# Kernel tuning notes

Measured on AMD Instinct MI355X. Metric: run time of the kernel, lower is better.

## Reference

```python
import jax, jax.numpy as jnp
import numpy as np

B, T, N = 16, 1024, 128
WIN, STEP = 30, 2
MOMENT_ORDERS = (2, 4, 8)
D_MODEL = 256


def _mask_diag(corr):
    n = corr.shape[-1]
    eye = jnp.eye(n, dtype=corr.dtype)
    return corr * (1.0 - eye) + eye


def corrcoef_time(xw):
    # xw: [..., L, N] -> corr over channels: [..., N, N]
    L = xw.shape[-2]
    xm = xw - xw.mean(axis=-2, keepdims=True)
    cov = jnp.einsum('...ln,...lm->...nm', xm, xm) / (L - 1 + 1e-8)
    var = jnp.clip(jnp.diagonal(cov, axis1=-2, axis2=-1), 1e-8, None)
    std = jnp.sqrt(var)
    corr = cov / (std[..., :, None] * std[..., None, :])
    corr = jnp.nan_to_num(corr, nan=0.0, posinf=0.0, neginf=0.0)
    return _mask_diag(corr)


def rowwise_corr(M):
    # M: [B, N, F]
    Xc = M - M.mean(axis=-1, keepdims=True)
    num = jnp.einsum('bnf,bmf->bnm', Xc, Xc)
    den1 = jnp.sqrt(jnp.clip((Xc ** 2).sum(axis=-1), 1e-8, None))
    corr = num / (den1[:, :, None] * den1[:, None, :])
    corr = jnp.nan_to_num(corr, nan=0.0, posinf=0.0, neginf=0.0)
    return _mask_diag(corr)


def layer_norm(x, gamma, beta, eps=1e-5):
    mu = x.mean(axis=-1, keepdims=True)
    var = ((x - mu) ** 2).mean(axis=-1, keepdims=True)
    return (x - mu) / jnp.sqrt(var + eps) * gamma + beta


def normalize_adj(adj):
    n = adj.shape[-1]
    A_hat = adj + jnp.eye(n, dtype=adj.dtype)
    d = A_hat.sum(axis=-1)
    dis = jnp.sqrt(1.0 / jnp.clip(d, 1e-8, None))
    return A_hat * dis[:, :, None] * dis[:, None, :]


def setup_inputs() -> dict:
    key = jax.random.key(0)
    ks = jax.random.split(key, 8)
    in_dim = len(MOMENT_ORDERS) * N
    return {
        'x': jax.random.normal(ks[0], (B, T, N), dtype=jnp.float32),
        'ln_gamma': jnp.ones((in_dim,), jnp.float32),
        'ln_beta': jnp.zeros((in_dim,), jnp.float32),
        'W1': jax.random.normal(ks[1], (in_dim, D_MODEL), jnp.float32) * 0.05,
        'b1': jnp.zeros((D_MODEL,), jnp.float32),
        'W2': jax.random.normal(ks[2], (D_MODEL, D_MODEL), jnp.float32) * 0.05,
        'b2': jnp.zeros((D_MODEL,), jnp.float32),
        'Wc': jax.random.normal(ks[3], (D_MODEL, 1), jnp.float32) * 0.05,
        'bc': jnp.zeros((1,), jnp.float32),
    }


def reference(x, ln_gamma, ln_beta, W1, b1, W2, b2, Wc, bc):
    # sliding windows (static indices)
    starts = np.arange(0, T - WIN + 1, STEP)
    idx = starts[:, None] + np.arange(WIN)[None, :]
    xw = x[:, idx, :]
    lo = corrcoef_time(xw)                            # [B, Wn, N, N]

    mean_lo = lo.mean(axis=1, keepdims=True)
    centered = lo - mean_lo
    cm_list, ho_list = [], []
    for d in MOMENT_ORDERS:
        cm = jnp.nan_to_num((centered ** d).mean(axis=1),
                            nan=0.0, posinf=0.0, neginf=0.0)  # [B, N, N]
        cm_list.append(cm)
        ho_list.append(rowwise_corr(cm))

    X = jnp.concatenate(cm_list, axis=-1)             # [B, N, 3N]
    X = layer_norm(X, ln_gamma, ln_beta)

    A = jnp.stack(ho_list, axis=1).mean(axis=1)
    A = 0.5 * (A + jnp.swapaxes(A, 1, 2))
    A_norm = normalize_adj(A)

    H = jax.nn.relu(jnp.einsum('bnm,bmd->bnd', A_norm, X @ W1 + b1))
    H = jax.nn.relu(jnp.einsum('bnm,bmd->bnd', A_norm, H @ W2 + b2))
    g = H.mean(axis=1)                                # [B, d_model]
    out = jax.nn.sigmoid(g @ Wc + bc)                 # [B, 1]
    return out
```

## Files before the change

kernel.cpp:

```cpp
#include <hip/hip_runtime.h>
#include <math.h>

#define BB  16
#define TT  1024
#define NN  128
#define WIN 30
#define NWD 498
#define DM  256
#define IND 384
#define GW  9

#define INV_W (1.0f/498.0f)

#define SARR (BB*NN*NN)

#define OFF_A     0
#define OFF_G     (OFF_A    + BB*NWD*NN)
#define OFF_CM2   (OFF_G    + BB*NWD*NN)
#define OFF_CM4   (OFF_CM2  + SARR)
#define OFF_CM8   (OFF_CM4  + SARR)
#define OFF_AD    (OFF_CM8  + SARR)
#define OFF_PART  (OFF_AD   + 3*SARR)
#define OFF_ANORM OFF_PART
#define OFF_BUFA  (OFF_ANORM + SARR)
#define OFF_BUFB  (OFF_BUFA + BB*NN*DM)

__global__ __launch_bounds__(128) void k1_stats(const float* __restrict__ x, float* __restrict__ ws) {
    int bx = blockIdx.x;
    int c = bx & 15, b = bx >> 4;
    int w0 = c*32, w1 = min(NWD, w0+32);
    int n = threadIdx.x;
    const float* xp = x + (size_t)b*TT*NN + n;

    float sum = 0.f, sq = 0.f;
    for (int t = 2*w0; t < 2*w0 + WIN; ++t) {
        float v = xp[(size_t)t*NN];
        sum += v; sq = fmaf(v, v, sq);
    }
    for (int w = w0; w < w1; ++w) {
        if (w > w0) {
            float o0 = xp[(size_t)(2*w-2)*NN], o1 = xp[(size_t)(2*w-1)*NN];
            float n0 = xp[(size_t)(2*w+28)*NN], n1 = xp[(size_t)(2*w+29)*NN];
            sum += (n0 + n1) - (o0 + o1);
            sq  += (n0*n0 + n1*n1) - (o0*o0 + o1*o1);
        }
        float mean = sum * (1.0f/30.0f);
        float ss = sq - 30.0f*mean*mean;
        float var = fmaxf(ss * (1.0f/29.0f), 1e-8f);
        float a = (1.0f / sqrtf(var)) * 0.185695338f;
        ws[OFF_A + ((size_t)b*NWD + w)*NN + n] = a;
        ws[OFF_G + ((size_t)b*NWD + w)*NN + n] = mean * a * 5.477225575f;
    }
}

__global__ __launch_bounds__(256) __attribute__((amdgpu_waves_per_eu(3, 3)))
void k24_inc(const float* __restrict__ x, float* __restrict__ ws) {
    __shared__ __align__(16) float xr[64][NN];
    __shared__ __align__(16) float sa[GW][NN];
    __shared__ __align__(16) float sg[GW][NN];
    int bx = blockIdx.x;
    int wc = bx & 7;
    int slab = (bx >> 3) % 6;
    int b = bx / 48;
    const char IS[6] = {0,0,0,0,1,1};
    const char JS[6] = {0,1,2,3,2,3};
    int is = IS[slab], js = JS[slab];
    int w0 = wc * 63, w1 = min(NWD, w0 + 63);
    int tid = threadIdx.x;
    int jg = tid & 7, ig = tid >> 3;
    int i0 = is*64 + ig*2;
    int j0 = js*32 + jg*4;

    const float* xb = x + (size_t)b*TT*NN;
    const float* Ab = ws + OFF_A + (size_t)b*NWD*NN;
    const float* Gb = ws + OFF_G + (size_t)b*NWD*NN;

    float P[2][4];
    float S1[2][4], S2[2][4], S3[2][4], S4[2][4], S5[2][4], S6[2][4], S7[2][4], S8[2][4];
#pragma unroll
    for (int p=0;p<2;++p)
#pragma unroll
        for (int q=0;q<4;++q) {
            P[p][q]=0.f;
            S1[p][q]=0.f;S2[p][q]=0.f;S3[p][q]=0.f;S4[p][q]=0.f;
            S5[p][q]=0.f;S6[p][q]=0.f;S7[p][q]=0.f;S8[p][q]=0.f;
        }

    auto moments = [&](int k) {
        float2 ai = *(const float2*)&sa[k][i0];
        float2 gi = *(const float2*)&sg[k][i0];
        float4 aj = *(const float4*)&sa[k][j0];
        float4 gj = *(const float4*)&sg[k][j0];
        float av[2] = {ai.x, ai.y};
        float mg[2] = {-gi.x, -gi.y};
        float aw[4] = {aj.x, aj.y, aj.z, aj.w};
        float gw[4] = {gj.x, gj.y, gj.z, gj.w};
#pragma unroll
        for (int p=0;p<2;++p)
#pragma unroll
            for (int q=0;q<4;++q) {
                float aa  = av[p]*aw[q];
                float ngg = mg[p]*gw[q];
                float c   = fmaf(P[p][q], aa, ngg);
                float c2 = c*c;
                float c3 = c2*c;
                float c4 = c2*c2;
                S1[p][q] += c;
                S2[p][q] += c2;
                S3[p][q] += c3;
                S4[p][q] += c4;
                S5[p][q] = fmaf(c4, c,  S5[p][q]);
                S6[p][q] = fmaf(c3, c3, S6[p][q]);
                S7[p][q] = fmaf(c3, c4, S7[p][q]);
                S8[p][q] = fmaf(c4, c4, S8[p][q]);
            }
    };

    int rlo = 2*w0;
    for (int wg = w0; wg < w1; wg += GW) {
        int m = min(GW, w1 - wg);
        __syncthreads();
        int rhi = 2*(wg + m - 1) + 29;
        int nr = rhi - rlo + 1;
        for (int idx = tid; idx < nr*32; idx += 256) {
            int r = idx >> 5, c4 = idx & 31;
            int t = rlo + r;
            *(float4*)&xr[t & 63][c4*4] = ((const float4*)(xb + (size_t)t*NN))[c4];
        }
        for (int idx = tid; idx < m*32; idx += 256) {
            int k = idx >> 5, c4 = idx & 31;
            *(float4*)&sa[k][c4*4] = ((const float4*)(Ab + (size_t)(wg+k)*NN))[c4];
        }
        for (int idx = tid; idx < m*32; idx += 256) {
            int k = idx >> 5, c4 = idx & 31;
            *(float4*)&sg[k][c4*4] = ((const float4*)(Gb + (size_t)(wg+k)*NN))[c4];
        }
        rlo = rhi + 1;
        __syncthreads();

        int kstart = 0;
        if (wg == w0) {
#pragma unroll 6
            for (int k = 0; k < WIN; ++k) {
                int t = 2*w0 + k;
                float2 xi = *(const float2*)&xr[t & 63][i0];
                float4 xj = *(const float4*)&xr[t & 63][j0];
                float av[2] = {xi.x, xi.y};
                float bv[4] = {xj.x, xj.y, xj.z, xj.w};
#pragma unroll
                for (int p=0;p<2;++p)
#pragma unroll
                    for (int q=0;q<4;++q) P[p][q] = fmaf(av[p], bv[q], P[p][q]);
            }
            moments(0);
            kstart = 1;
        }
        for (int k = kstart; k < m; ++k) {
            int w = wg + k;
            int tr[4] = {2*w - 2, 2*w - 1, 2*w + 28, 2*w + 29};
#pragma unroll
            for (int kk = 0; kk < 4; ++kk) {
                int t = tr[kk];
                float sgn = (kk < 2) ? -1.0f : 1.0f;
                float2 xi = *(const float2*)&xr[t & 63][i0];
                float4 xj = *(const float4*)&xr[t & 63][j0];
                float av[2] = {sgn*xi.x, sgn*xi.y};
                float bv[4] = {xj.x, xj.y, xj.z, xj.w};
#pragma unroll
                for (int p=0;p<2;++p)
#pragma unroll
                    for (int q=0;q<4;++q) P[p][q] = fmaf(av[p], bv[q], P[p][q]);
            }
            moments(k);
        }
    }

    float* tp = ws + OFF_PART + (size_t)bx*16384 + tid*8;
#define STORE_ARR(A, S) \
    *(float4*)&tp[(A)*2048]     = make_float4(S[0][0], S[0][1], S[0][2], S[0][3]); \
    *(float4*)&tp[(A)*2048 + 4] = make_float4(S[1][0], S[1][1], S[1][2], S[1][3]);
    STORE_ARR(0, S1) STORE_ARR(1, S2) STORE_ARR(2, S3) STORE_ARR(3, S4)
    STORE_ARR(4, S5) STORE_ARR(5, S6) STORE_ARR(6, S7) STORE_ARR(7, S8)
#undef STORE_ARR
}

__global__ __launch_bounds__(256) void kred(float* __restrict__ ws) {
    int pair = blockIdx.x >> 3, sub = blockIdx.x & 7;
    int b = pair / 6, slab = pair % 6;
    const char IS[6] = {0,0,0,0,1,1};
    const char JS[6] = {0,1,2,3,2,3};
    int is = IS[slab], js = JS[slab];
    int off = sub*256 + threadIdx.x;
    const float* base = ws + OFF_PART + (size_t)(b*48 + slab*8)*16384;

    float E[8];
#pragma unroll
    for (int a=0;a<8;++a) E[a] = 0.f;
    for (int c = 0; c < 8; ++c) {
        const float* tp = base + (size_t)c*16384;
#pragma unroll
        for (int a=0;a<8;++a) E[a] += tp[a*2048 + off];
    }

    int tid_old = off >> 3, e = off & 7;
    int ig = tid_old >> 3, jg = tid_old & 7;
    int p = e >> 2, q = e & 3;
    int i = is*64 + ig*2 + p;
    int j = js*32 + jg*4 + q;

    float cm2, cm4, cm8;
    if (i == j) {
        cm2 = 0.f; cm4 = 0.f; cm8 = 0.f;
    } else {
        float e1 = E[0]*INV_W, e2 = E[1]*INV_W, e3 = E[2]*INV_W, e4 = E[3]*INV_W;
        float e5 = E[4]*INV_W, e6 = E[5]*INV_W, e7 = E[6]*INV_W, e8 = E[7]*INV_W;
        float m  = e1;
        float m2 = m*m, m3 = m2*m, m4 = m2*m2, m5 = m4*m, m6 = m3*m3, m8 = m4*m4;
        cm2 = e2 - m2;
        cm4 = e4 - 4.f*m*e3 + 6.f*m2*e2 - 3.f*m4;
        cm8 = e8 - 8.f*m*e7 + 28.f*m2*e6 - 56.f*m3*e5 + 70.f*m4*e4
                 - 56.f*m5*e3 + 28.f*m6*e2 - 7.f*m8;
    }
    float* C2 = ws + OFF_CM2 + (size_t)b*NN*NN;
    float* C4 = ws + OFF_CM4 + (size_t)b*NN*NN;
    float* C8 = ws + OFF_CM8 + (size_t)b*NN*NN;
    C2[i*NN + j] = cm2; C2[j*NN + i] = cm2;
    C4[i*NN + j] = cm4; C4[j*NN + i] = cm4;
    C8[i*NN + j] = cm8; C8[j*NN + i] = cm8;
}

__global__ __launch_bounds__(256) void kB(const float* __restrict__ gamma, const float* __restrict__ beta,
                                          const float* __restrict__ W1, const float* __restrict__ b1,
                                          float* __restrict__ ws) {
    __shared__ __align__(16) float smem[NN*(NN+1) + 2*NN];
    int blk = blockIdx.x, tid = threadIdx.x;
    if (blk < 192) {
        int rem = blk % 12;
        int b = blk / 12, di = rem >> 2, jq = rem & 3;
        float* Xc  = smem;
        float* rmn = smem + NN*(NN+1);
        float* iden = rmn + NN;
        const float* cm = ws + (di==0 ? OFF_CM2 : (di==1 ? OFF_CM4 : OFF_CM8)) + (size_t)b*NN*NN;
        for (int idx = tid; idx < NN*NN; idx += 256) {
            int n = idx >> 7, f = idx & 127;
            Xc[n*(NN+1)+f] = cm[idx];
        }
        __syncthreads();
        if (tid < NN) {
            float s = 0.f;
            for (int f = 0; f < NN; ++f) s += Xc[tid*(NN+1)+f];
            rmn[tid] = s * (1.0f/NN);
        }
        __syncthreads();
        for (int idx = tid; idx < NN*NN; idx += 256) {
            int n = idx >> 7, f = idx & 127;
            Xc[n*(NN+1)+f] -= rmn[n];
        }
        __syncthreads();
        if (tid < NN) {
            float s = 0.f;
            for (int f = 0; f < NN; ++f) { float v = Xc[tid*(NN+1)+f]; s = fmaf(v, v, s); }
            iden[tid] = 1.0f/sqrtf(fmaxf(s, 1e-8f));
        }
        __syncthreads();
        int n0 = (tid >> 4)*8, m0 = jq*32 + (tid & 15)*2;
        float acc[8][2];
#pragma unroll
        for (int k=0;k<8;++k) { acc[k][0]=0.f; acc[k][1]=0.f; }
        for (int f = 0; f < NN; ++f) {
            float am0 = Xc[(m0  )*(NN+1)+f];
            float am1 = Xc[(m0+1)*(NN+1)+f];
#pragma unroll
            for (int k=0;k<8;++k) {
                float an = Xc[(n0+k)*(NN+1)+f];
                acc[k][0] = fmaf(an, am0, acc[k][0]);
                acc[k][1] = fmaf(an, am1, acc[k][1]);
            }
        }
        float* Ad = ws + OFF_AD + (size_t)(b*3 + di)*NN*NN;
#pragma unroll
        for (int k=0;k<8;++k)
#pragma unroll
            for (int l=0;l<2;++l) {
                int gi = n0+k, gj = m0+l;
                float v = acc[k][l]*iden[gi]*iden[gj];
                if (gi == gj) v = 1.0f;
                Ad[gi*NN + gj] = v;
            }
    } else {
        int r0 = (blk - 192) * 8;
        float* Xs = smem;
        float* sm = smem + 8*IND;
        float* sr = sm + 8;
        for (int r = 0; r < 8; ++r) {
            int row = r0 + r;
            int b = row >> 7, n = row & 127;
            const float* c2 = ws + OFF_CM2 + ((size_t)b*NN + n)*NN;
            const float* c4 = ws + OFF_CM4 + ((size_t)b*NN + n)*NN;
            const float* c8 = ws + OFF_CM8 + ((size_t)b*NN + n)*NN;
            for (int c = tid; c < IND; c += 256)
                Xs[r*IND+c] = (c < 128) ? c2[c] : (c < 256) ? c4[c-128] : c8[c-256];
        }
        __syncthreads();
        {
            int team = tid >> 5, lane = tid & 31;
            float s = 0.f;
            for (int c = lane; c < IND; c += 32) s += Xs[team*IND + c];
#pragma unroll
            for (int o = 16; o > 0; o >>= 1) s += __shfl_down(s, o, 32);
            float mean = __shfl(s, 0, 32) * (1.0f/IND);
            float v = 0.f;
            for (int c = lane; c < IND; c += 32) { float d = Xs[team*IND + c] - mean; v = fmaf(d, d, v); }
#pragma unroll
            for (int o = 16; o > 0; o >>= 1) v += __shfl_down(v, o, 32);
            if (lane == 0) {
                sm[team] = mean;
                sr[team] = 1.0f / sqrtf(v*(1.0f/IND) + 1e-5f);
            }
        }
        __syncthreads();
        for (int r = 0; r < 8; ++r) {
            float mean = sm[r], rstd = sr[r];
            for (int c = tid; c < IND; c += 256)
                Xs[r*IND+c] = (Xs[r*IND+c] - mean)*rstd*gamma[c] + beta[c];
        }
        __syncthreads();
        float acc[8];
        float bv = b1[tid];
#pragma unroll
        for (int r = 0; r < 8; ++r) acc[r] = bv;
#pragma unroll 4
        for (int k = 0; k < IND; ++k) {
            float wv = W1[(size_t)k*DM + tid];
#pragma unroll
            for (int r = 0; r < 8; ++r) acc[r] = fmaf(Xs[r*IND+k], wv, acc[r]);
        }
        float* O = ws + OFF_BUFA;
#pragma unroll
        for (int r = 0; r < 8; ++r) O[(size_t)(r0+r)*DM + tid] = acc[r];
    }
}

__global__ __launch_bounds__(256) void k6_anorm(float* __restrict__ ws) {
    __shared__ float As[NN][NN+1];
    __shared__ float dis[NN];
    int b = blockIdx.x;
    const float* A0 = ws + OFF_AD + (size_t)(b*3 + 0)*NN*NN;
    const float* A1 = ws + OFF_AD + (size_t)(b*3 + 1)*NN*NN;
    const float* A2 = ws + OFF_AD + (size_t)(b*3 + 2)*NN*NN;
    int tid = threadIdx.x;
    for (int idx = tid; idx < NN*NN; idx += 256) {
        int n = idx >> 7, m = idx & 127;
        int ji = m*NN + n;
        float s = A0[idx] + A0[ji] + A1[idx] + A1[ji] + A2[idx] + A2[ji];
        As[n][m] = s * (1.0f/6.0f);
    }
    __syncthreads();
    if (tid < NN) {
        float d = 1.0f;
        for (int m = 0; m < NN; ++m) d += As[tid][m];
        dis[tid] = sqrtf(1.0f / fmaxf(d, 1e-8f));
    }
    __syncthreads();
    float* An = ws + OFF_ANORM + (size_t)b*NN*NN;
    for (int idx = tid; idx < NN*NN; idx += 256) {
        int n = idx >> 7, m = idx & 127;
        float v = As[n][m] + (n==m ? 1.0f : 0.0f);
        An[idx] = v * dis[n] * dis[m];
    }
}

__global__ __launch_bounds__(256) void k98_propgemm(const float* __restrict__ W2, const float* __restrict__ b2,
                                                    float* __restrict__ ws) {
    __shared__ float Ar[8][NN];
    __shared__ float Hs[8][DM];
    int bx = blockIdx.x;
    int b = bx >> 4, n0 = (bx & 15)*8;
    int tid = threadIdx.x;
    const float* A = ws + OFF_ANORM + (size_t)b*NN*NN;
    if (tid < NN) {
#pragma unroll
        for (int r = 0; r < 8; ++r) Ar[r][tid] = A[(n0+r)*NN + tid];
    }
    __syncthreads();
    float acc[8] = {0,0,0,0,0,0,0,0};
    const float* Z = ws + OFF_BUFA + (size_t)b*NN*DM;
#pragma unroll 4
    for (int m = 0; m < NN; ++m) {
        float z = Z[(size_t)m*DM + tid];
#pragma unroll
        for (int r = 0; r < 8; ++r) acc[r] = fmaf(Ar[r][m], z, acc[r]);
    }
#pragma unroll
    for (int r = 0; r < 8; ++r) Hs[r][tid] = fmaxf(acc[r], 0.0f);
    __syncthreads();
    float acc2[8];
    float bv = b2[tid];
#pragma unroll
    for (int r = 0; r < 8; ++r) acc2[r] = bv;
#pragma unroll 4
    for (int k = 0; k < DM; ++k) {
        float wv = W2[(size_t)k*DM + tid];
#pragma unroll
        for (int r = 0; r < 8; ++r) acc2[r] = fmaf(Hs[r][k], wv, acc2[r]);
    }
    float* O = ws + OFF_BUFB + (size_t)b*NN*DM;
#pragma unroll
    for (int r = 0; r < 8; ++r) O[(size_t)(n0+r)*DM + tid] = acc2[r];
}

__global__ __launch_bounds__(256) void k9_prop(float* __restrict__ ws) {
    __shared__ float Ar[8][NN];
    int bx = blockIdx.x;
    int b = bx >> 4, n0 = (bx & 15)*8;
    int tid = threadIdx.x;
    const float* A = ws + OFF_ANORM + (size_t)b*NN*NN;
    if (tid < NN) {
#pragma unroll
        for (int r = 0; r < 8; ++r) Ar[r][tid] = A[(n0+r)*NN + tid];
    }
    __syncthreads();
    float acc[8] = {0,0,0,0,0,0,0,0};
    const float* Z = ws + OFF_BUFB + (size_t)b*NN*DM;
#pragma unroll 4
    for (int m = 0; m < NN; ++m) {
        float z = Z[(size_t)m*DM + tid];
#pragma unroll
        for (int r = 0; r < 8; ++r) acc[r] = fmaf(Ar[r][m], z, acc[r]);
    }
    float* O = ws + OFF_BUFA + (size_t)b*NN*DM;
#pragma unroll
    for (int r = 0; r < 8; ++r) O[(size_t)(n0+r)*DM + tid] = fmaxf(acc[r], 0.0f);
}

__global__ __launch_bounds__(256) void k12_head(const float* __restrict__ Wc, const float* __restrict__ bc,
                                                float* __restrict__ ws, float* __restrict__ outp) {
    __shared__ float red[256];
    int b = blockIdx.x, tid = threadIdx.x;
    const float* H = ws + OFF_BUFA + (size_t)b*NN*DM;
    float s = 0.f;
    for (int n = 0; n < NN; ++n) s += H[(size_t)n*DM + tid];
    red[tid] = s * (1.0f/NN) * Wc[tid];
    __syncthreads();
    for (int o = 128; o > 0; o >>= 1) { if (tid < o) red[tid] += red[tid+o]; __syncthreads(); }
    if (tid == 0) outp[b] = 1.0f/(1.0f + expf(-(red[0] + bc[0])));
}

extern "C" void kernel_launch(void* const* d_in, const int* in_sizes, int n_in,
                              void* d_out, int out_size, void* d_ws, size_t ws_size,
                              hipStream_t stream) {
    (void)in_sizes; (void)n_in; (void)out_size; (void)ws_size;
    const float* x     = (const float*)d_in[0];
    const float* gamma = (const float*)d_in[1];
    const float* beta  = (const float*)d_in[2];
    const float* W1    = (const float*)d_in[3];
    const float* b1    = (const float*)d_in[4];
    const float* W2    = (const float*)d_in[5];
    const float* b2    = (const float*)d_in[6];
    const float* Wc    = (const float*)d_in[7];
    const float* bc    = (const float*)d_in[8];
    float* ws  = (float*)d_ws;
    float* out = (float*)d_out;

    k1_stats   <<<BB*16,   128, 0, stream>>>(x, ws);
    k24_inc    <<<BB*6*8,  256, 0, stream>>>(x, ws);
    kred       <<<BB*6*8,  256, 0, stream>>>(ws);
    kB         <<<448,     256, 0, stream>>>(gamma, beta, W1, b1, ws);
    k6_anorm   <<<BB,      256, 0, stream>>>(ws);
    k98_propgemm<<<BB*16,  256, 0, stream>>>(W2, b2, ws);
    k9_prop    <<<BB*16,   256, 0, stream>>>(ws);
    k12_head   <<<BB,      256, 0, stream>>>(Wc, bc, ws, out);
}
```

Measured before the change: 264.1 us.

## Fuse reduction, anorm and head into producers via last-block-done atomic counters

Removes three kernel launches (kred, k6_anorm, k12_head) by having the last block to finish in each group, found through an atomic counter, perform the downstream reduction or epilogue. Counters are zeroed in k1_stats. This is meant to cut launch gaps and tail overhead between the small kernels. In exchange, the reduction, anorm and head work is serialized onto one block per group instead of being spread across many blocks, which can lengthen the tail. The scheme also depends on acquire/release atomics for memory visibility.

Result: slower. 305.4 us (+15.6%).

```diff
diff --git a/kernel.cpp b/kernel.cpp
--- a/kernel.cpp
+++ b/kernel.cpp
@@ -24,9 +24,11 @@
 #define OFF_ANORM OFF_PART
 #define OFF_BUFA  (OFF_ANORM + SARR)
 #define OFF_BUFB  (OFF_BUFA + BB*NN*DM)
+#define OFF_CTR   (OFF_PART + 768*16384)
 
 __global__ __launch_bounds__(128) void k1_stats(const float* __restrict__ x, float* __restrict__ ws) {
     int bx = blockIdx.x;
+    if (bx == 0 && threadIdx.x < 128) ((unsigned*)(ws + OFF_CTR))[threadIdx.x] = 0u;
     int c = bx & 15, b = bx >> 4;
     int w0 = c*32, w1 = min(NWD, w0+32);
     int n = threadIdx.x;
@@ -58,6 +60,7 @@
     __shared__ __align__(16) float xr[64][NN];
     __shared__ __align__(16) float sa[GW][NN];
     __shared__ __align__(16) float sg[GW][NN];
+    __shared__ unsigned iswin;
     int bx = blockIdx.x;
     int wc = bx & 7;
     int slab = (bx >> 3) % 6;
@@ -182,57 +185,59 @@
     STORE_ARR(0, S1) STORE_ARR(1, S2) STORE_ARR(2, S3) STORE_ARR(3, S4)
     STORE_ARR(4, S5) STORE_ARR(5, S6) STORE_ARR(6, S7) STORE_ARR(7, S8)
 #undef STORE_ARR
-}
-
-__global__ __launch_bounds__(256) void kred(float* __restrict__ ws) {
-    int pair = blockIdx.x >> 3, sub = blockIdx.x & 7;
-    int b = pair / 6, slab = pair % 6;
-    const char IS[6] = {0,0,0,0,1,1};
-    const char JS[6] = {0,1,2,3,2,3};
-    int is = IS[slab], js = JS[slab];
-    int off = sub*256 + threadIdx.x;
-    const float* base = ws + OFF_PART + (size_t)(b*48 + slab*8)*16384;
-
-    float E[8];
-#pragma unroll
-    for (int a=0;a<8;++a) E[a] = 0.f;
-    for (int c = 0; c < 8; ++c) {
-        const float* tp = base + (size_t)c*16384;
-#pragma unroll
-        for (int a=0;a<8;++a) E[a] += tp[a*2048 + off];
-    }
-
-    int tid_old = off >> 3, e = off & 7;
-    int ig = tid_old >> 3, jg = tid_old & 7;
-    int p = e >> 2, q = e & 3;
-    int i = is*64 + ig*2 + p;
-    int j = js*32 + jg*4 + q;
-
-    float cm2, cm4, cm8;
-    if (i == j) {
-        cm2 = 0.f; cm4 = 0.f; cm8 = 0.f;
-    } else {
-        float e1 = E[0]*INV_W, e2 = E[1]*INV_W, e3 = E[2]*INV_W, e4 = E[3]*INV_W;
-        float e5 = E[4]*INV_W, e6 = E[5]*INV_W, e7 = E[6]*INV_W, e8 = E[7]*INV_W;
-        float m  = e1;
-        float m2 = m*m, m3 = m2*m, m4 = m2*m2, m5 = m4*m, m6 = m3*m3, m8 = m4*m4;
-        cm2 = e2 - m2;
-        cm4 = e4 - 4.f*m*e3 + 6.f*m2*e2 - 3.f*m4;
-        cm8 = e8 - 8.f*m*e7 + 28.f*m2*e6 - 56.f*m3*e5 + 70.f*m4*e4
-                 - 56.f*m5*e3 + 28.f*m6*e2 - 7.f*m8;
-    }
-    float* C2 = ws + OFF_CM2 + (size_t)b*NN*NN;
-    float* C4 = ws + OFF_CM4 + (size_t)b*NN*NN;
-    float* C8 = ws + OFF_CM8 + (size_t)b*NN*NN;
-    C2[i*NN + j] = cm2; C2[j*NN + i] = cm2;
-    C4[i*NN + j] = cm4; C4[j*NN + i] = cm4;
-    C8[i*NN + j] = cm8; C8[j*NN + i] = cm8;
+
+    __syncthreads();
+    if (tid == 0) {
+        unsigned* ctr = (unsigned*)(ws + OFF_CTR);
+        unsigned old = __hip_atomic_fetch_add(&ctr[b*6 + slab], 1u,
+                                              __ATOMIC_ACQ_REL, __HIP_MEMORY_SCOPE_AGENT);
+        iswin = (old == 7u) ? 1u : 0u;
+    }
+    __syncthreads();
+    if (iswin) {
+        const float* base = ws + OFF_PART + (size_t)(b*48 + slab*8)*16384;
+        float* C2 = ws + OFF_CM2 + (size_t)b*NN*NN;
+        float* C4 = ws + OFF_CM4 + (size_t)b*NN*NN;
+        float* C8 = ws + OFF_CM8 + (size_t)b*NN*NN;
+        for (int k = 0; k < 8; ++k) {
+            int off = k*256 + tid;
+            float E[8];
+#pragma unroll
+            for (int a=0;a<8;++a) E[a] = 0.f;
+            for (int c = 0; c < 8; ++c) {
+                const float* tpp = base + (size_t)c*16384;
+#pragma unroll
+                for (int a=0;a<8;++a) E[a] += tpp[a*2048 + off];
+            }
+            int tid_old = off >> 3, e = off & 7;
+            int igo = tid_old >> 3, jgo = tid_old & 7;
+            int p = e >> 2, q = e & 3;
+            int i = is*64 + igo*2 + p;
+            int j = js*32 + jgo*4 + q;
+            float cm2, cm4, cm8;
+            if (i == j) { cm2 = 0.f; cm4 = 0.f; cm8 = 0.f; }
+            else {
+                float e1 = E[0]*INV_W, e2 = E[1]*INV_W, e3 = E[2]*INV_W, e4 = E[3]*INV_W;
+                float e5 = E[4]*INV_W, e6 = E[5]*INV_W, e7 = E[6]*INV_W, e8 = E[7]*INV_W;
+                float m  = e1;
+                float m2 = m*m, m3 = m2*m, m4 = m2*m2, m5 = m4*m, m6 = m3*m3, m8 = m4*m4;
+                cm2 = e2 - m2;
+                cm4 = e4 - 4.f*m*e3 + 6.f*m2*e2 - 3.f*m4;
+                cm8 = e8 - 8.f*m*e7 + 28.f*m2*e6 - 56.f*m3*e5 + 70.f*m4*e4
+                         - 56.f*m5*e3 + 28.f*m6*e2 - 7.f*m8;
+            }
+            C2[i*NN + j] = cm2; C2[j*NN + i] = cm2;
+            C4[i*NN + j] = cm4; C4[j*NN + i] = cm4;
+            C8[i*NN + j] = cm8; C8[j*NN + i] = cm8;
+        }
+    }
 }
 
 __global__ __launch_bounds__(256) void kB(const float* __restrict__ gamma, const float* __restrict__ beta,
                                           const float* __restrict__ W1, const float* __restrict__ b1,
                                           float* __restrict__ ws) {
     __shared__ __align__(16) float smem[NN*(NN+1) + 2*NN];
+    __shared__ unsigned winB;
     int blk = blockIdx.x, tid = threadIdx.x;
     if (blk < 192) {
         int rem = blk % 12;
@@ -287,6 +292,41 @@
                 if (gi == gj) v = 1.0f;
                 Ad[gi*NN + gj] = v;
             }
+
+        __syncthreads();
+        if (tid == 0) {
+            unsigned* ctr = (unsigned*)(ws + OFF_CTR);
+            unsigned old = __hip_atomic_fetch_add(&ctr[96 + b], 1u,
+                                                  __ATOMIC_ACQ_REL, __HIP_MEMORY_SCOPE_AGENT);
+            winB = (old == 11u) ? 1u : 0u;
+        }
+        __syncthreads();
+        if (winB) {
+            float* As = smem;
+            float* dis = smem + NN*(NN+1);
+            const float* A0 = ws + OFF_AD + (size_t)(b*3 + 0)*NN*NN;
+            const float* A1 = ws + OFF_AD + (size_t)(b*3 + 1)*NN*NN;
+            const float* A2 = ws + OFF_AD + (size_t)(b*3 + 2)*NN*NN;
+            for (int idx = tid; idx < NN*NN; idx += 256) {
+                int n = idx >> 7, m = idx & 127;
+                int ji = m*NN + n;
+                float s = A0[idx] + A0[ji] + A1[idx] + A1[ji] + A2[idx] + A2[ji];
+                As[n*(NN+1)+m] = s * (1.0f/6.0f);
+            }
+            __syncthreads();
+            if (tid < NN) {
+                float d = 1.0f;
+                for (int m = 0; m < NN; ++m) d += As[tid*(NN+1)+m];
+                dis[tid] = sqrtf(1.0f / fmaxf(d, 1e-8f));
+            }
+            __syncthreads();
+            float* An = ws + OFF_ANORM + (size_t)b*NN*NN;
+            for (int idx = tid; idx < NN*NN; idx += 256) {
+                int n = idx >> 7, m = idx & 127;
+                float v = As[n*(NN+1)+m] + (n==m ? 1.0f : 0.0f);
+                An[idx] = v * dis[n] * dis[m];
+            }
+        }
     } else {
         int r0 = (blk - 192) * 8;
         float* Xs = smem;
@@ -341,35 +381,6 @@
     }
 }
 
-__global__ __launch_bounds__(256) void k6_anorm(float* __restrict__ ws) {
-    __shared__ float As[NN][NN+1];
-    __shared__ float dis[NN];
-    int b = blockIdx.x;
-    const float* A0 = ws + OFF_AD + (size_t)(b*3 + 0)*NN*NN;
-    const float* A1 = ws + OFF_AD + (size_t)(b*3 + 1)*NN*NN;
-    const float* A2 = ws + OFF_AD + (size_t)(b*3 + 2)*NN*NN;
-    int tid = threadIdx.x;
-    for (int idx = tid; idx < NN*NN; idx += 256) {
-        int n = idx >> 7, m = idx & 127;
-        int ji = m*NN + n;
-        float s = A0[idx] + A0[ji] + A1[idx] + A1[ji] + A2[idx] + A2[ji];
-        As[n][m] = s * (1.0f/6.0f);
-    }
-    __syncthreads();
-    if (tid < NN) {
-        float d = 1.0f;
-        for (int m = 0; m < NN; ++m) d += As[tid][m];
-        dis[tid] = sqrtf(1.0f / fmaxf(d, 1e-8f));
-    }
-    __syncthreads();
-    float* An = ws + OFF_ANORM + (size_t)b*NN*NN;
-    for (int idx = tid; idx < NN*NN; idx += 256) {
-        int n = idx >> 7, m = idx & 127;
-        float v = As[n][m] + (n==m ? 1.0f : 0.0f);
-        An[idx] = v * dis[n] * dis[m];
-    }
-}
-
 __global__ __launch_bounds__(256) void k98_propgemm(const float* __restrict__ W2, const float* __restrict__ b2,
                                                     float* __restrict__ ws) {
     __shared__ float Ar[8][NN];
@@ -409,8 +420,11 @@
     for (int r = 0; r < 8; ++r) O[(size_t)(n0+r)*DM + tid] = acc2[r];
 }
 
-__global__ __launch_bounds__(256) void k9_prop(float* __restrict__ ws) {
+__global__ __launch_bounds__(256) void k9_prop(const float* __restrict__ Wc, const float* __restrict__ bc,
+                                               float* __restrict__ ws, float* __restrict__ outp) {
     __shared__ float Ar[8][NN];
+    __shared__ float red[256];
+    __shared__ unsigned win9;
     int bx = blockIdx.x;
     int b = bx >> 4, n0 = (bx & 15)*8;
     int tid = threadIdx.x;
@@ -431,19 +445,24 @@
     float* O = ws + OFF_BUFA + (size_t)b*NN*DM;
 #pragma unroll
     for (int r = 0; r < 8; ++r) O[(size_t)(n0+r)*DM + tid] = fmaxf(acc[r], 0.0f);
-}
-
-__global__ __launch_bounds__(256) void k12_head(const float* __restrict__ Wc, const float* __restrict__ bc,
-                                                float* __restrict__ ws, float* __restrict__ outp) {
-    __shared__ float red[256];
-    int b = blockIdx.x, tid = threadIdx.x;
-    const float* H = ws + OFF_BUFA + (size_t)b*NN*DM;
-    float s = 0.f;
-    for (int n = 0; n < NN; ++n) s += H[(size_t)n*DM + tid];
-    red[tid] = s * (1.0f/NN) * Wc[tid];
-    __syncthreads();
-    for (int o = 128; o > 0; o >>= 1) { if (tid < o) red[tid] += red[tid+o]; __syncthreads(); }
-    if (tid == 0) outp[b] = 1.0f/(1.0f + expf(-(red[0] + bc[0])));
+
+    __syncthreads();
+    if (tid == 0) {
+        unsigned* ctr = (unsigned*)(ws + OFF_CTR);
+        unsigned old = __hip_atomic_fetch_add(&ctr[112 + b], 1u,
+                                              __ATOMIC_ACQ_REL, __HIP_MEMORY_SCOPE_AGENT);
+        win9 = (old == 15u) ? 1u : 0u;
+    }
+    __syncthreads();
+    if (win9) {
+        const float* H = ws + OFF_BUFA + (size_t)b*NN*DM;
+        float s = 0.f;
+        for (int n = 0; n < NN; ++n) s += H[(size_t)n*DM + tid];
+        red[tid] = s * (1.0f/NN) * Wc[tid];
+        __syncthreads();
+        for (int o = 128; o > 0; o >>= 1) { if (tid < o) red[tid] += red[tid+o]; __syncthreads(); }
+        if (tid == 0) outp[b] = 1.0f/(1.0f + expf(-(red[0] + bc[0])));
+    }
 }
 
 extern "C" void kernel_launch(void* const* d_in, const int* in_sizes, int n_in,
@@ -462,12 +481,9 @@
     float* ws  = (float*)d_ws;
     float* out = (float*)d_out;
 
-    k1_stats   <<<BB*16,   128, 0, stream>>>(x, ws);
-    k24_inc    <<<BB*6*8,  256, 0, stream>>>(x, ws);
-    kred       <<<BB*6*8,  256, 0, stream>>>(ws);
-    kB         <<<448,     256, 0, stream>>>(gamma, beta, W1, b1, ws);
-    k6_anorm   <<<BB,      256, 0, stream>>>(ws);
+    k1_stats    <<<BB*16,  128, 0, stream>>>(x, ws);
+    k24_inc     <<<BB*6*8, 256, 0, stream>>>(x, ws);
+    kB          <<<448,    256, 0, stream>>>(gamma, beta, W1, b1, ws);
     k98_propgemm<<<BB*16,  256, 0, stream>>>(W2, b2, ws);
-    k9_prop    <<<BB*16,   256, 0, stream>>>(ws);
-    k12_head   <<<BB,      256, 0, stream>>>(Wc, bc, ws, out);
-}
+    k9_prop     <<<BB*16,  256, 0, stream>>>(Wc, bc, ws, out);
+}
```
